# Optimization experiments

Measured on AMD Instinct MI355X. Metric: run time of the kernel, lower is better.

The kernel has to match this reference:

```python
import jax, jax.numpy as jnp
import numpy as np

ALPHA = 0.2  # LeakyReLU negative slope
NEG_INF = -9e15


def setup_inputs() -> dict:
    key = jax.random.key(0)
    k1, k2, k3, k4 = jax.random.split(key, 4)
    B, N, Fin, Fout = 8, 2048, 128, 64
    inp = jax.random.normal(k1, (B, N, Fin), dtype=jnp.float32)
    # sparse-ish binary adjacency (avg degree ~32)
    adj = (jax.random.uniform(k2, (B, N, N)) < (32.0 / N)).astype(jnp.int32)
    # xavier_uniform with gain=1.414
    limW = 1.414 * np.sqrt(6.0 / (Fin + Fout))
    W = jax.random.uniform(k3, (Fin, Fout), minval=-limW, maxval=limW, dtype=jnp.float32)
    lima = 1.414 * np.sqrt(6.0 / (2 * Fout + 1))
    a = jax.random.uniform(k4, (2 * Fout, 1), minval=-lima, maxval=lima, dtype=jnp.float32)
    return {"input": inp, "adj": adj, "W": W, "a": a}


def reference(input, adj, W, a):
    # h: [B, N, Fout]
    h = jnp.matmul(input, W)
    Fout = W.shape[1]
    a1 = a[:Fout, 0]   # coefficient on h_i (row)
    a2 = a[Fout:, 0]   # coefficient on h_j (col)
    f1 = jnp.einsum('bnf,f->bn', h, a1)  # [B, N]
    f2 = jnp.einsum('bnf,f->bn', h, a2)  # [B, N]
    # e[b,i,j] = LeakyReLU(a1.h_i + a2.h_j) -- no [B,N,N,2F] intermediate
    e = jax.nn.leaky_relu(f1[:, :, None] + f2[:, None, :], negative_slope=ALPHA)
    attn = jnp.where(adj > 0, e, NEG_INF)
    # NOTE: original softmax over dim=1 (normalizes over source rows i for each column j)
    attn = jax.nn.softmax(attn, axis=1)
    # dropout p=0.0 (eval reference) -> identity
    h_prime = jnp.matmul(attn, h)  # [B, N, Fout]
    return jax.nn.elu(h_prime)     # concat=True path
```

## Files before the change

kernel.cpp:

```cpp
#include <hip/hip_runtime.h>
#include <math.h>

#define BB 8
#define NN 2048
#define ROWS (BB * NN)
#define FIN 128
#define FOUT 64
#define GAT_ALPHA 0.2f
#define CAP 128

__device__ __forceinline__ float lrelu(float x) { return x > 0.f ? x : GAT_ALPHA * x; }

__global__ __launch_bounds__(256) void k1_gemm(
        const float* __restrict__ inp, const float* __restrict__ W,
        const float* __restrict__ a, float* __restrict__ h,
        float* __restrict__ f1, float* __restrict__ f2,
        float* __restrict__ colsum, float* __restrict__ emptysum) {
    const int tid  = blockIdx.x * 256 + threadIdx.x;
    const int lane = threadIdx.x & 63;
    const int w    = tid >> 6;
    if (tid < ROWS) colsum[tid] = 0.f;
    if (tid < BB * FOUT) emptysum[tid] = 0.f;

    const float* i0 = inp + (size_t)w * FIN;
    const float* i1 = i0 + (size_t)4096 * FIN;
    const float* i2 = i0 + (size_t)8192 * FIN;
    const float* i3 = i0 + (size_t)12288 * FIN;
    float c0 = 0.f, c1 = 0.f, c2 = 0.f, c3 = 0.f;
    #pragma unroll 8
    for (int k = 0; k < FIN; ++k) {
        float wk = W[k * FOUT + lane];
        c0 = fmaf(i0[k], wk, c0);
        c1 = fmaf(i1[k], wk, c1);
        c2 = fmaf(i2[k], wk, c2);
        c3 = fmaf(i3[k], wk, c3);
    }
    h[(size_t)w * FOUT + lane]           = c0;
    h[((size_t)w + 4096) * FOUT + lane]  = c1;
    h[((size_t)w + 8192) * FOUT + lane]  = c2;
    h[((size_t)w + 12288) * FOUT + lane] = c3;

    float aa = a[lane], ab = a[FOUT + lane];
    float p0 = c0 * aa, q0 = c0 * ab, p1 = c1 * aa, q1 = c1 * ab;
    float p2 = c2 * aa, q2 = c2 * ab, p3 = c3 * aa, q3 = c3 * ab;
    #pragma unroll
    for (int off = 32; off; off >>= 1) {
        p0 += __shfl_xor(p0, off, 64); q0 += __shfl_xor(q0, off, 64);
        p1 += __shfl_xor(p1, off, 64); q1 += __shfl_xor(q1, off, 64);
        p2 += __shfl_xor(p2, off, 64); q2 += __shfl_xor(q2, off, 64);
        p3 += __shfl_xor(p3, off, 64); q3 += __shfl_xor(q3, off, 64);
    }
    if (lane == 0) {
        f1[w] = p0;          f2[w] = q0;
        f1[w + 4096] = p1;   f2[w + 4096] = q1;
        f1[w + 8192] = p2;   f2[w + 8192] = q2;
        f1[w + 12288] = p3;  f2[w + 12288] = q3;
    }
}

__global__ __launch_bounds__(256) void k2_scan(
        const int* __restrict__ adj, const float* __restrict__ f1,
        const float* __restrict__ f2, unsigned short* __restrict__ lists,
        int* __restrict__ rowcnt, float* __restrict__ colsum) {
    const int gtid = blockIdx.x * 256 + threadIdx.x;
    const int row  = gtid >> 6;
    const int lane = threadIdx.x & 63;
    const int b    = row >> 11;
    const unsigned long long lmask_lt = (1ull << lane) - 1ull;
    const float f1i = f1[row];
    const int4* arow = (const int4*)(adj + (size_t)row * NN);
    const float* f2b = f2 + (b << 11);
    float* csb = colsum + (b << 11);
    unsigned short* lr = lists + (size_t)row * CAP;
    int cnt = 0;
    #pragma unroll
    for (int it = 0; it < NN / 256; ++it) {
        int4 v = arow[it * 64 + lane];
        int jb = (it * 64 + lane) * 4;
        #pragma unroll
        for (int e = 0; e < 4; ++e) {
            int val = (e == 0) ? v.x : (e == 1) ? v.y : (e == 2) ? v.z : v.w;
            bool nz = (val != 0);
            unsigned long long m = __ballot(nz);
            if (nz) {
                int j = jb + e;
                int pos = cnt + __popcll(m & lmask_lt);
                if (pos < CAP) lr[pos] = (unsigned short)j;
                atomicAdd(&csb[j], expf(lrelu(f1i + f2b[j])));
            }
            cnt += __popcll(m);
        }
    }
    if (lane == 0) rowcnt[row] = min(cnt, CAP);
}

__global__ __launch_bounds__(256) void k3b_empty(
        const float* __restrict__ colsum, const float* __restrict__ h,
        float* __restrict__ emptysum) {
    int c = blockIdx.x * 256 + threadIdx.x;
    if (c >= ROWS) return;
    if (colsum[c] == 0.f) {
        int b = c >> 11;
        const float* hr = h + (size_t)c * FOUT;
        for (int f = 0; f < FOUT; ++f)
            atomicAdd(&emptysum[b * FOUT + f], hr[f] * (1.0f / NN));
    }
}

__global__ __launch_bounds__(256) void k4_out(
        const unsigned short* __restrict__ lists, const int* __restrict__ rowcnt,
        const float* __restrict__ f1, const float* __restrict__ f2,
        const float* __restrict__ colsum, const float* __restrict__ h,
        const float* __restrict__ emptysum, float* __restrict__ out) {
    const int gtid = blockIdx.x * 256 + threadIdx.x;
    const int row  = gtid >> 6;
    const int lane = threadIdx.x & 63;
    const int b    = row >> 11;
    const int cnt  = rowcnt[row];
    const float f1i = f1[row];
    const unsigned short* lr = lists + (size_t)row * CAP;
    float acc = 0.f;
    for (int t = 0; t < cnt; ++t) {
        int c = (b << 11) + lr[t];
        float wgt = expf(lrelu(f1i + f2[c])) / colsum[c];
        acc = fmaf(wgt, h[(size_t)c * FOUT + lane], acc);
    }
    acc += emptysum[b * FOUT + lane];
    out[(size_t)row * FOUT + lane] = acc > 0.f ? acc : expm1f(acc);
}

extern "C" void kernel_launch(void* const* d_in, const int* in_sizes, int n_in,
                              void* d_out, int out_size, void* d_ws, size_t ws_size,
                              hipStream_t stream) {
    const float* inp = (const float*)d_in[0];
    const int*   adj = (const int*)d_in[1];
    const float* W   = (const float*)d_in[2];
    const float* a   = (const float*)d_in[3];
    float* out = (float*)d_out;

    char* ws = (char*)d_ws;
    float*          h        = (float*)(ws);
    unsigned short* lists    = (unsigned short*)(ws + 4194304);
    float*          f1       = (float*)(ws + 8388608);
    float*          f2       = (float*)(ws + 8454144);
    float*          colsum   = (float*)(ws + 8519680);
    int*            rowcnt   = (int*)(ws + 8585216);
    float*          emptysum = (float*)(ws + 8650752);

    k1_gemm<<<1024, 256, 0, stream>>>(inp, W, a, h, f1, f2, colsum, emptysum);
    k2_scan<<<4096, 256, 0, stream>>>(adj, f1, f2, lists, rowcnt, colsum);
    k3b_empty<<<ROWS / 256, 256, 0, stream>>>(colsum, h, emptysum);
    k4_out<<<4096, 256, 0, stream>>>(lists, rowcnt, f1, f2, colsum, h,
                                     emptysum, out);
}
```

Before: 313.4 us.

## Replace per-element ballots with bitmask prefix scan and parallelize edge weights

The adjacency scan now loads all eight int4 chunks up front, builds a per-lane 32-bit nonzero mask, and uses a wave-level shfl_up prefix sum to place list entries. This replaces 32 serialized ballot/popcount steps per row. The output kernel computes each edge's softmax weight once per lane, in parallel across the wave, and broadcasts it with shuffles. That removes redundant per-lane exp, divide and gather work, and four independent accumulators add memory-level parallelism. Neighbor list order changes, which alters atomic and summation ordering and can shift floating-point results slightly.

```diff
diff --git a/kernel.cpp b/kernel.cpp
--- a/kernel.cpp
+++ b/kernel.cpp
@@ -66,32 +66,44 @@
     const int row  = gtid >> 6;
     const int lane = threadIdx.x & 63;
     const int b    = row >> 11;
-    const unsigned long long lmask_lt = (1ull << lane) - 1ull;
     const float f1i = f1[row];
-    const int4* arow = (const int4*)(adj + (size_t)row * NN);
+    const int4* a4 = (const int4*)(adj + (size_t)row * NN);
     const float* f2b = f2 + (b << 11);
     float* csb = colsum + (b << 11);
     unsigned short* lr = lists + (size_t)row * CAP;
-    int cnt = 0;
+
+    int4 v0 = a4[lane];       int4 v1 = a4[64 + lane];
+    int4 v2 = a4[128 + lane]; int4 v3 = a4[192 + lane];
+    int4 v4 = a4[256 + lane]; int4 v5 = a4[320 + lane];
+    int4 v6 = a4[384 + lane]; int4 v7 = a4[448 + lane];
+
+    unsigned mask = 0u;
+    #define ACCM(v, base) \
+        mask |= ((v.x != 0) ? 1u : 0u) << (base); \
+        mask |= ((v.y != 0) ? 1u : 0u) << ((base) + 1); \
+        mask |= ((v.z != 0) ? 1u : 0u) << ((base) + 2); \
+        mask |= ((v.w != 0) ? 1u : 0u) << ((base) + 3);
+    ACCM(v0, 0)  ACCM(v1, 4)  ACCM(v2, 8)  ACCM(v3, 12)
+    ACCM(v4, 16) ACCM(v5, 20) ACCM(v6, 24) ACCM(v7, 28)
+    #undef ACCM
+
+    int my = __popc(mask);
+    int sc = my;
     #pragma unroll
-    for (int it = 0; it < NN / 256; ++it) {
-        int4 v = arow[it * 64 + lane];
-        int jb = (it * 64 + lane) * 4;
-        #pragma unroll
-        for (int e = 0; e < 4; ++e) {
-            int val = (e == 0) ? v.x : (e == 1) ? v.y : (e == 2) ? v.z : v.w;
-            bool nz = (val != 0);
-            unsigned long long m = __ballot(nz);
-            if (nz) {
-                int j = jb + e;
-                int pos = cnt + __popcll(m & lmask_lt);
-                if (pos < CAP) lr[pos] = (unsigned short)j;
-                atomicAdd(&csb[j], expf(lrelu(f1i + f2b[j])));
-            }
-            cnt += __popcll(m);
-        }
-    }
-    if (lane == 0) rowcnt[row] = min(cnt, CAP);
+    for (int off = 1; off < 64; off <<= 1) {
+        int n = __shfl_up(sc, off, 64);
+        if (lane >= off) sc += n;
+    }
+    int pos = sc - my;
+    unsigned m = mask;
+    while (m) {
+        int t = __ffs(m) - 1; m &= m - 1;
+        int j = ((t >> 2) << 8) + (lane << 2) + (t & 3);
+        if (pos < CAP) lr[pos] = (unsigned short)j;
+        atomicAdd(&csb[j], expf(lrelu(f1i + f2b[j])));
+        ++pos;
+    }
+    if (lane == 63) rowcnt[row] = min(sc, CAP);
 }
 
 __global__ __launch_bounds__(256) void k3b_empty(
@@ -119,13 +131,47 @@
     const int cnt  = rowcnt[row];
     const float f1i = f1[row];
     const unsigned short* lr = lists + (size_t)row * CAP;
-    float acc = 0.f;
-    for (int t = 0; t < cnt; ++t) {
-        int c = (b << 11) + lr[t];
-        float wgt = expf(lrelu(f1i + f2[c])) / colsum[c];
-        acc = fmaf(wgt, h[(size_t)c * FOUT + lane], acc);
-    }
-    acc += emptysum[b * FOUT + lane];
+    const float* f2b = f2 + (b << 11);
+    const float* csb = colsum + (b << 11);
+    const float* hb  = h + ((size_t)(b << 11)) * FOUT;
+
+    int   j_lo = 0; float w_lo = 0.f;
+    if (lane < cnt) {
+        j_lo = lr[lane];
+        w_lo = expf(lrelu(f1i + f2b[j_lo])) / csb[j_lo];
+    }
+    int   j_hi = 0; float w_hi = 0.f;
+    if (cnt > 64 && lane + 64 < cnt) {
+        j_hi = lr[lane + 64];
+        w_hi = expf(lrelu(f1i + f2b[j_hi])) / csb[j_hi];
+    }
+
+    const int c4 = (cnt + 3) & ~3;
+    float a0 = 0.f, a1 = 0.f, a2 = 0.f, a3 = 0.f;
+    const int lo = c4 < 64 ? c4 : 64;
+    for (int t = 0; t < lo; t += 4) {
+        int   j0 = __shfl(j_lo, t, 64),     j1 = __shfl(j_lo, t + 1, 64);
+        int   j2 = __shfl(j_lo, t + 2, 64), j3 = __shfl(j_lo, t + 3, 64);
+        float w0 = __shfl(w_lo, t, 64),     w1 = __shfl(w_lo, t + 1, 64);
+        float w2 = __shfl(w_lo, t + 2, 64), w3 = __shfl(w_lo, t + 3, 64);
+        a0 = fmaf(w0, hb[(size_t)j0 * FOUT + lane], a0);
+        a1 = fmaf(w1, hb[(size_t)j1 * FOUT + lane], a1);
+        a2 = fmaf(w2, hb[(size_t)j2 * FOUT + lane], a2);
+        a3 = fmaf(w3, hb[(size_t)j3 * FOUT + lane], a3);
+    }
+    if (c4 > 64) {
+        for (int t = 64; t < c4; t += 4) {
+            int   j0 = __shfl(j_hi, t - 64, 64), j1 = __shfl(j_hi, t - 63, 64);
+            int   j2 = __shfl(j_hi, t - 62, 64), j3 = __shfl(j_hi, t - 61, 64);
+            float w0 = __shfl(w_hi, t - 64, 64), w1 = __shfl(w_hi, t - 63, 64);
+            float w2 = __shfl(w_hi, t - 62, 64), w3 = __shfl(w_hi, t - 61, 64);
+            a0 = fmaf(w0, hb[(size_t)j0 * FOUT + lane], a0);
+            a1 = fmaf(w1, hb[(size_t)j1 * FOUT + lane], a1);
+            a2 = fmaf(w2, hb[(size_t)j2 * FOUT + lane], a2);
+            a3 = fmaf(w3, hb[(size_t)j3 * FOUT + lane], a3);
+        }
+    }
+    float acc = ((a0 + a1) + (a2 + a3)) + emptysum[b * FOUT + lane];
     out[(size_t)row * FOUT + lane] = acc > 0.f ? acc : expm1f(acc);
 }
 
```

New measurement: 251.9 us. 19.6% less time.
